# Performance work log

Measured on AMD Instinct MI355X. Metric: run time of the kernel, lower is better.

Reference implementation:

```python
import jax, jax.numpy as jnp
import numpy as np

HIDDEN = 2048
N_HEADS = 16
HEAD_DIM = HIDDEN // N_HEADS  # 128
BATCH = 2
SEQ = 2048


def setup_inputs() -> dict:
    key = jax.random.key(0)
    ks = jax.random.split(key, 9)
    std = HIDDEN ** -0.5
    inp = {
        "hidden_states": jax.random.normal(ks[0], (BATCH, SEQ, HIDDEN), dtype=jnp.float32),
        "q_w": jax.random.normal(ks[1], (HIDDEN, HIDDEN), dtype=jnp.float32) * std,
        "k_w": jax.random.normal(ks[2], (HIDDEN, HIDDEN), dtype=jnp.float32) * std,
        "v_w": jax.random.normal(ks[3], (HIDDEN, HIDDEN), dtype=jnp.float32) * std,
        "o_w": jax.random.normal(ks[4], (HIDDEN, HIDDEN), dtype=jnp.float32) * std,
        "q_b": jnp.zeros((HIDDEN,), dtype=jnp.float32),
        "k_b": jnp.zeros((HIDDEN,), dtype=jnp.float32),
        "v_b": jnp.zeros((HIDDEN,), dtype=jnp.float32),
        "o_b": jnp.zeros((HIDDEN,), dtype=jnp.float32),
    }
    return inp


def reference(hidden_states, q_w, k_w, v_w, o_w, q_b, k_b, v_b, o_b):
    b, s, _ = hidden_states.shape
    # Projections (nn.Linear applies x @ W^T + b); split heads -> [b, h, s, d]
    def proj(w, bias):
        y = hidden_states @ w.T + bias
        return y.reshape(b, s, N_HEADS, HEAD_DIM).transpose(0, 2, 1, 3)

    q = proj(q_w, q_b)
    k = proj(k_w, k_b)
    v = proj(v_w, v_b)

    scale = 1.0 / jnp.sqrt(jnp.float32(HEAD_DIM))
    scores = jnp.einsum("bhqd,bhkd->bhqk", q, k) * scale  # [b, h, s, s]

    # causal mask: mask positions where k > q (triu, diagonal=1)
    qi = jnp.arange(s)[:, None]
    ki = jnp.arange(s)[None, :]
    scores = jnp.where(ki > qi, -jnp.inf, scores)

    attn = jax.nn.softmax(scores.astype(jnp.float32), axis=-1).astype(q.dtype)
    out = jnp.einsum("bhqk,bhkd->bhqd", attn, v)
    out = out.transpose(0, 2, 1, 3).reshape(b, s, HIDDEN)
    return out @ o_w.T + o_b
```

## Files before the change

### kernel.cpp

```cpp
#include <hip/hip_runtime.h>

#define S_HID 2048
#define S_SEQ 2048
#define S_B   2
#define S_NH  16
#define S_HD  128
#define S_M   (S_B * S_SEQ)
#define S_BH  (S_B * S_NH)

typedef __bf16 bf16_t;
typedef __bf16 bf16x8 __attribute__((ext_vector_type(8)));
typedef __bf16 bf16x4 __attribute__((ext_vector_type(4)));
typedef float  floatx4 __attribute__((ext_vector_type(4)));
typedef float  floatx16 __attribute__((ext_vector_type(16)));

typedef __attribute__((address_space(1))) unsigned int as1_uint;
typedef __attribute__((address_space(3))) unsigned int as3_uint;

__device__ __forceinline__ void gload_lds16(const void* g, void* l) {
    __builtin_amdgcn_global_load_lds((as1_uint*)g, (as3_uint*)l, 16, 0, 0);
}

__global__ void cvt_all(const float* __restrict__ x,
                        const float* __restrict__ qw, const float* __restrict__ kw,
                        const float* __restrict__ vw, const float* __restrict__ ow,
                        bf16_t* __restrict__ Xb, bf16_t* __restrict__ Wqkv) {
    const int XV = (S_M * S_HID) >> 2;
    const int WV = (S_HID * S_HID) >> 2;
    const int total = XV + 4 * WV;
    int stride = gridDim.x * blockDim.x;
    for (int i = blockIdx.x * blockDim.x + threadIdx.x; i < total; i += stride) {
        const float* src;
        bf16x4* dst;
        int local;
        if (i < XV) {
            src = x; local = i; dst = (bf16x4*)Xb;
        } else {
            int j = i - XV;
            int r = j >> 20;
            local = j & (WV - 1);
            src = r == 0 ? qw : r == 1 ? kw : r == 2 ? vw : ow;
            dst = (bf16x4*)Wqkv + (size_t)r * WV;
        }
        float4 v = ((const float4*)src)[local];
        bf16x4 o;
        o.x = (bf16_t)v.x; o.y = (bf16_t)v.y; o.z = (bf16_t)v.z; o.w = (bf16_t)v.w;
        dst[local] = o;
    }
}

__global__ __launch_bounds__(256, 4)
void gemm_qkv(const bf16_t* __restrict__ A, const bf16_t* __restrict__ W,
              const float* __restrict__ qbias, const float* __restrict__ kbias,
              const float* __restrict__ vbias,
              bf16_t* __restrict__ Qo, bf16_t* __restrict__ Ko, bf16_t* __restrict__ Vto,
              float qscale) {
    __shared__ __align__(16) bf16_t ldsA[128 * 64];
    __shared__ __align__(16) bf16_t ldsB[128 * 64];
    const int tid = threadIdx.x;
    const int wid = tid >> 6, lane = tid & 63;
    const int m0 = blockIdx.y * 128, n0 = blockIdx.x * 128;
    const int wm = (wid & 1) * 64, wn = (wid >> 1) * 64;
    const int lm = lane & 15, quad = lane >> 4;
    const int srow = lane >> 3;
    const int scol = lane & 7;

    floatx4 acc[4][4];
    #pragma unroll
    for (int i = 0; i < 4; ++i)
        #pragma unroll
        for (int j = 0; j < 4; ++j)
            acc[i][j] = (floatx4){0.f, 0.f, 0.f, 0.f};

    for (int kt = 0; kt < S_HID; kt += 64) {
        #pragma unroll
        for (int i = 0; i < 4; ++i) {
            int slot = i * 4 + wid;
            int row = slot * 8 + srow;
            int cg = scol ^ (row & 7);
            gload_lds16(A + (size_t)(m0 + row) * S_HID + kt + cg * 8, &ldsA[slot * 512]);
            gload_lds16(W + (size_t)(n0 + row) * S_HID + kt + cg * 8, &ldsB[slot * 512]);
        }
        __syncthreads();
        #pragma unroll
        for (int k2 = 0; k2 < 2; ++k2) {
            bf16x8 af[4], bfr[4];
            #pragma unroll
            for (int i = 0; i < 4; ++i) {
                int row = wm + i * 16 + lm;
                int cc = (k2 * 4 + quad) ^ (row & 7);
                af[i] = *(const bf16x8*)&ldsA[row * 64 + cc * 8];
            }
            #pragma unroll
            for (int j = 0; j < 4; ++j) {
                int row = wn + j * 16 + lm;
                int cc = (k2 * 4 + quad) ^ (row & 7);
                bfr[j] = *(const bf16x8*)&ldsB[row * 64 + cc * 8];
            }
            #pragma unroll
            for (int i = 0; i < 4; ++i)
                #pragma unroll
                for (int j = 0; j < 4; ++j)
                    acc[i][j] = __builtin_amdgcn_mfma_f32_16x16x32_bf16(af[i], bfr[j], acc[i][j], 0, 0, 0);
        }
        __syncthreads();
    }

    const int region = n0 >> 11;
    if (region < 2) {
        bf16_t* Ob = region ? Ko : Qo;
        const float* bias = region ? kbias : qbias;
        float scale = region ? 1.0f : qscale;
        #pragma unroll
        for (int i = 0; i < 4; ++i) {
            #pragma unroll
            for (int j = 0; j < 4; ++j) {
                int n = n0 + wn + j * 16 + lm;
                float bv = bias[n & 2047];
                int nl = n & 2047;
                int h = nl >> 7, d = nl & 127;
                #pragma unroll
                for (int r = 0; r < 4; ++r) {
                    int m = m0 + wm + i * 16 + quad * 4 + r;
                    int b = m >> 11, s = m & 2047;
                    Ob[(((size_t)(b * S_NH + h)) * S_SEQ + s) * S_HD + d] =
                        (bf16_t)((acc[i][j][r] + bv) * scale);
                }
            }
        }
    } else {
        #pragma unroll
        for (int i = 0; i < 4; ++i) {
            #pragma unroll
            for (int j = 0; j < 4; ++j) {
                int n = n0 + wn + j * 16 + lm;
                int nl = n & 2047;
                float bv = vbias[nl];
                int h = nl >> 7, d = nl & 127;
                int m = m0 + wm + i * 16 + quad * 4;
                int b = m >> 11, s = m & 2047;
                bf16x4 ov;
                #pragma unroll
                for (int r = 0; r < 4; ++r) ov[r] = (bf16_t)(acc[i][j][r] + bv);
                *(bf16x4*)&Vto[(((size_t)(b * S_NH + h)) * S_HD + d) * S_SEQ + s] = ov;
            }
        }
    }
}

__global__ __launch_bounds__(256, 3)
void gemm_out(const bf16_t* __restrict__ A, const bf16_t* __restrict__ W,
              const float* __restrict__ bias, float* __restrict__ out) {
    __shared__ __align__(16) bf16_t ldsA[128 * 64];
    __shared__ __align__(16) bf16_t ldsB[128 * 64];
    const int tid = threadIdx.x;
    const int wid = tid >> 6, lane = tid & 63;
    const int m0 = blockIdx.y * 128, n0 = blockIdx.x * 128;
    const int wm = (wid & 1) * 64, wn = (wid >> 1) * 64;
    const int lm = lane & 15, quad = lane >> 4;
    const int srow = lane >> 3;
    const int scol = lane & 7;

    floatx4 acc[4][4];
    #pragma unroll
    for (int i = 0; i < 4; ++i)
        #pragma unroll
        for (int j = 0; j < 4; ++j)
            acc[i][j] = (floatx4){0.f, 0.f, 0.f, 0.f};

    for (int kt = 0; kt < S_HID; kt += 64) {
        #pragma unroll
        for (int i = 0; i < 4; ++i) {
            int slot = i * 4 + wid;
            int row = slot * 8 + srow;
            int cg = scol ^ (row & 7);
            gload_lds16(A + (size_t)(m0 + row) * S_HID + kt + cg * 8, &ldsA[slot * 512]);
            gload_lds16(W + (size_t)(n0 + row) * S_HID + kt + cg * 8, &ldsB[slot * 512]);
        }
        __syncthreads();
        #pragma unroll
        for (int k2 = 0; k2 < 2; ++k2) {
            bf16x8 af[4], bfr[4];
            #pragma unroll
            for (int i = 0; i < 4; ++i) {
                int row = wm + i * 16 + lm;
                int cc = (k2 * 4 + quad) ^ (row & 7);
                af[i] = *(const bf16x8*)&ldsA[row * 64 + cc * 8];
            }
            #pragma unroll
            for (int j = 0; j < 4; ++j) {
                int row = wn + j * 16 + lm;
                int cc = (k2 * 4 + quad) ^ (row & 7);
                bfr[j] = *(const bf16x8*)&ldsB[row * 64 + cc * 8];
            }
            #pragma unroll
            for (int i = 0; i < 4; ++i)
                #pragma unroll
                for (int j = 0; j < 4; ++j)
                    acc[i][j] = __builtin_amdgcn_mfma_f32_16x16x32_bf16(af[i], bfr[j], acc[i][j], 0, 0, 0);
        }
        __syncthreads();
    }

    #pragma unroll
    for (int i = 0; i < 4; ++i) {
        #pragma unroll
        for (int j = 0; j < 4; ++j) {
            int n = n0 + wn + j * 16 + lm;
            float bv = bias[n];
            #pragma unroll
            for (int r = 0; r < 4; ++r) {
                int m = m0 + wm + i * 16 + quad * 4 + r;
                out[(size_t)m * S_HID + n] = acc[i][j][r] + bv;
            }
        }
    }
}

__device__ __forceinline__ bf16x8 make_pfrag(bf16x4 lo, bf16x4 hi, int h) {
    int2 li = __builtin_bit_cast(int2, lo);
    int2 hh = __builtin_bit_cast(int2, hi);
    int2 xl, xh;
    xl.x = __shfl_xor(li.x, 32); xl.y = __shfl_xor(li.y, 32);
    xh.x = __shfl_xor(hh.x, 32); xh.y = __shfl_xor(hh.y, 32);
    int2 flo, fhi;
    flo.x = h ? xh.x : li.x;  flo.y = h ? xh.y : li.y;
    fhi.x = h ? hh.x : xl.x;  fhi.y = h ? hh.y : xl.y;
    bf16x4 a = __builtin_bit_cast(bf16x4, flo);
    bf16x4 b = __builtin_bit_cast(bf16x4, fhi);
    return __builtin_shufflevector(a, b, 0, 1, 2, 3, 4, 5, 6, 7);
}

__global__ __launch_bounds__(256, 2)
void attn(const bf16_t* __restrict__ Q, const bf16_t* __restrict__ K,
          const bf16_t* __restrict__ Vt, bf16_t* __restrict__ O) {
    __shared__ __align__(16) bf16_t ldsK[2][64 * 128];
    __shared__ __align__(16) bf16_t ldsV[2][128 * 64];
    const int tid = threadIdx.x, wid = tid >> 6, lane = tid & 63;
    const int lm = lane & 15, quad = lane >> 4;
    const int srow = lane >> 3, scol = lane & 7;
    const int c31 = lane & 31, h = lane >> 5, r7 = lane & 7;
    const int bx = blockIdx.x;
    const int bh = bx & 31, idx = bx >> 5;
    const int qt = idx < 8 ? idx : 23 - idx;
    const int q0 = qt * 128;
    const int b = bh >> 4, hd = bh & 15;

    const bf16_t* Kbase = K + (size_t)bh * S_SEQ * S_HD;
    const bf16_t* Vbase = Vt + (size_t)bh * S_HD * S_SEQ;

    const int qcol = q0 + wid * 32 + c31;
    const int nkt = qt * 2 + 2;

    bf16x8 qf[8];
    {
        const bf16_t* qp = Q + ((size_t)bh * S_SEQ + qcol) * S_HD + h * 8;
        #pragma unroll
        for (int ks = 0; ks < 8; ++ks) qf[ks] = *(const bf16x8*)(qp + ks * 16);
    }

    floatx16 oa[4];
    #pragma unroll
    for (int jd = 0; jd < 4; ++jd)
        #pragma unroll
        for (int e = 0; e < 16; ++e) oa[jd][e] = 0.f;
    float m_st = -1e30f, l_st = 0.f;

    #pragma unroll
    for (int i = 0; i < 4; ++i) {
        int slot = i * 4 + wid;
        int krow = slot * 4 + quad;
        int kcg = lm ^ (krow & 7);
        gload_lds16(Kbase + (size_t)krow * S_HD + kcg * 8, &ldsK[0][slot * 512]);
        int vrow = slot * 8 + srow;
        int vcg = scol ^ (vrow & 7);
        gload_lds16(Vbase + (size_t)vrow * S_SEQ + vcg * 8, &ldsV[0][slot * 512]);
    }

    int pp = 0;
    for (int kti = 0; kti < nkt; ++kti) {
        const int kt = kti * 64;
        __syncthreads();

        if (kti + 1 < nkt) {
            const int ktn = kt + 64;
            #pragma unroll
            for (int i = 0; i < 4; ++i) {
                int slot = i * 4 + wid;
                int krow = slot * 4 + quad;
                int kcg = lm ^ (krow & 7);
                gload_lds16(Kbase + (size_t)(ktn + krow) * S_HD + kcg * 8, &ldsK[pp ^ 1][slot * 512]);
                int vrow = slot * 8 + srow;
                int vcg = scol ^ (vrow & 7);
                gload_lds16(Vbase + (size_t)vrow * S_SEQ + ktn + vcg * 8, &ldsV[pp ^ 1][slot * 512]);
            }
        }

        floatx16 sa[2];
        #pragma unroll
        for (int jr = 0; jr < 2; ++jr)
            #pragma unroll
            for (int e = 0; e < 16; ++e) sa[jr][e] = 0.f;
        __builtin_amdgcn_s_setprio(1);
        #pragma unroll
        for (int ks = 0; ks < 8; ++ks) {
            #pragma unroll
            for (int jr = 0; jr < 2; ++jr) {
                int row = jr * 32 + c31;
                bf16x8 kf = *(const bf16x8*)&ldsK[pp][row * 128 + (((ks * 2 + h) ^ r7)) * 8];
                sa[jr] = __builtin_amdgcn_mfma_f32_32x32x16_bf16(kf, qf[ks], sa[jr], 0, 0, 0);
            }
        }
        __builtin_amdgcn_s_setprio(0);

        if (kti >= nkt - 2) {
            #pragma unroll
            for (int jr = 0; jr < 2; ++jr)
                #pragma unroll
                for (int rr = 0; rr < 16; ++rr) {
                    int key = kt + jr * 32 + (rr & 3) + 8 * (rr >> 2) + 4 * h;
                    if (key > qcol) sa[jr][rr] = -1e30f;
                }
        }

        float mx = -1e30f;
        #pragma unroll
        for (int jr = 0; jr < 2; ++jr)
            #pragma unroll
            for (int rr = 0; rr < 16; ++rr) mx = fmaxf(mx, sa[jr][rr]);
        mx = fmaxf(mx, __shfl_xor(mx, 32));
        float mn = fmaxf(m_st, mx);
        float al = __builtin_amdgcn_exp2f(m_st - mn);
        m_st = mn;

        float rs = 0.f;
        bf16x8 pf[4];
        #pragma unroll
        for (int jr = 0; jr < 2; ++jr) {
            bf16x4 pk[4];
            #pragma unroll
            for (int g = 0; g < 4; ++g)
                #pragma unroll
                for (int e = 0; e < 4; ++e) {
                    float p = __builtin_amdgcn_exp2f(sa[jr][g * 4 + e] - mn);
                    rs += p;
                    pk[g][e] = (bf16_t)p;
                }
            pf[jr * 2]     = make_pfrag(pk[0], pk[1], h);
            pf[jr * 2 + 1] = make_pfrag(pk[2], pk[3], h);
        }
        rs += __shfl_xor(rs, 32);
        l_st = l_st * al + rs;
        #pragma unroll
        for (int jd = 0; jd < 4; ++jd)
            #pragma unroll
            for (int e = 0; e < 16; ++e) oa[jd][e] *= al;

        __builtin_amdgcn_s_setprio(1);
        #pragma unroll
        for (int kb = 0; kb < 4; ++kb) {
            #pragma unroll
            for (int jd = 0; jd < 4; ++jd) {
                int row = jd * 32 + c31;
                bf16x8 vf = *(const bf16x8*)&ldsV[pp][row * 64 + (((kb * 2 + h) ^ r7)) * 8];
                oa[jd] = __builtin_amdgcn_mfma_f32_32x32x16_bf16(vf, pf[kb], oa[jd], 0, 0, 0);
            }
        }
        __builtin_amdgcn_s_setprio(0);
        pp ^= 1;
    }

    float inv = 1.0f / l_st;
    bf16_t* op = O + ((size_t)b * S_SEQ + qcol) * S_HID + hd * S_HD;
    #pragma unroll
    for (int jd = 0; jd < 4; ++jd)
        #pragma unroll
        for (int g = 0; g < 4; ++g) {
            bf16x4 ov;
            #pragma unroll
            for (int e = 0; e < 4; ++e) ov[e] = (bf16_t)(oa[jd][g * 4 + e] * inv);
            *(bf16x4*)&op[jd * 32 + g * 8 + 4 * h] = ov;
        }
}

extern "C" void kernel_launch(void* const* d_in, const int* in_sizes, int n_in,
                              void* d_out, int out_size, void* d_ws, size_t ws_size,
                              hipStream_t stream) {
    const float* hs = (const float*)d_in[0];
    const float* qw = (const float*)d_in[1];
    const float* kw = (const float*)d_in[2];
    const float* vw = (const float*)d_in[3];
    const float* ow = (const float*)d_in[4];
    const float* qbias = (const float*)d_in[5];
    const float* kbias = (const float*)d_in[6];
    const float* vbias = (const float*)d_in[7];
    const float* obias = (const float*)d_in[8];

    char* ws = (char*)d_ws;
    bf16_t* Xb   = (bf16_t*)(ws + 0);
    bf16_t* Wqkv = (bf16_t*)(ws + 16777216);
    bf16_t* Wob  = (bf16_t*)(ws + 41943040);
    bf16_t* Qb   = (bf16_t*)(ws + 50331648);
    bf16_t* Kb   = (bf16_t*)(ws + 67108864);
    bf16_t* Vtb  = (bf16_t*)(ws + 83886080);
    bf16_t* Ob   = Xb;

    cvt_all<<<2048, 256, 0, stream>>>(hs, qw, kw, vw, ow, Xb, Wqkv);

    const float qscale = 0.08838834764831845f * 1.4426950408889634f;
    gemm_qkv<<<dim3(48, 32), 256, 0, stream>>>(Xb, Wqkv, qbias, kbias, vbias,
                                               Qb, Kb, Vtb, qscale);

    attn<<<512, 256, 0, stream>>>(Qb, Kb, Vtb, Ob);

    gemm_out<<<dim3(16, 32), 256, 0, stream>>>(Ob, Wob, obias, (float*)d_out);
}
```

Before: 360.7 us.

## Triple-buffer QKV GEMM with 128x256 tiles and lazy softmax rescale in attention

The QKV projection GEMM moves to 512-thread blocks computing 128x256 tiles. A three-stage LDS ring buffer prefetches two K-steps ahead, the loads are interleaved across half-steps, and MFMA bursts run at raised priority. This is meant to overlap global loads with matrix math and cut the per-K-step full-sync stalls. Separately, the attention softmax skips the running-max update and the output rescale unless some lane's max grows by more than 8 in log2 units. That saves the rescale multiplies at the cost of slightly larger intermediate exponent values.

```diff
diff --git a/kernel.cpp b/kernel.cpp
--- a/kernel.cpp
+++ b/kernel.cpp
@@ -49,21 +49,23 @@
     }
 }
 
-__global__ __launch_bounds__(256, 4)
+__global__ __launch_bounds__(512, 2)
 void gemm_qkv(const bf16_t* __restrict__ A, const bf16_t* __restrict__ W,
               const float* __restrict__ qbias, const float* __restrict__ kbias,
               const float* __restrict__ vbias,
               bf16_t* __restrict__ Qo, bf16_t* __restrict__ Ko, bf16_t* __restrict__ Vto,
               float qscale) {
-    __shared__ __align__(16) bf16_t ldsA[128 * 64];
-    __shared__ __align__(16) bf16_t ldsB[128 * 64];
+    __shared__ __align__(16) bf16_t ldsA[3][128 * 64];
+    __shared__ __align__(16) bf16_t ldsB[3][256 * 64];
     const int tid = threadIdx.x;
     const int wid = tid >> 6, lane = tid & 63;
-    const int m0 = blockIdx.y * 128, n0 = blockIdx.x * 128;
-    const int wm = (wid & 1) * 64, wn = (wid >> 1) * 64;
+    const int wr = wid >> 2, wc = wid & 3;
     const int lm = lane & 15, quad = lane >> 4;
-    const int srow = lane >> 3;
-    const int scol = lane & 7;
+    const int srow = lane >> 3, scol = lane & 7;
+    const int m0 = blockIdx.y * 128, n0 = blockIdx.x * 256;
+
+    const bf16_t* Ag = A + (size_t)m0 * S_HID;
+    const bf16_t* Wg = W + (size_t)n0 * S_HID;
 
     floatx4 acc[4][4];
     #pragma unroll
@@ -72,39 +74,76 @@
         for (int j = 0; j < 4; ++j)
             acc[i][j] = (floatx4){0.f, 0.f, 0.f, 0.f};
 
-    for (int kt = 0; kt < S_HID; kt += 64) {
-        #pragma unroll
-        for (int i = 0; i < 4; ++i) {
-            int slot = i * 4 + wid;
-            int row = slot * 8 + srow;
-            int cg = scol ^ (row & 7);
-            gload_lds16(A + (size_t)(m0 + row) * S_HID + kt + cg * 8, &ldsA[slot * 512]);
-            gload_lds16(W + (size_t)(n0 + row) * S_HID + kt + cg * 8, &ldsB[slot * 512]);
-        }
-        __syncthreads();
-        #pragma unroll
-        for (int k2 = 0; k2 < 2; ++k2) {
-            bf16x8 af[4], bfr[4];
-            #pragma unroll
-            for (int i = 0; i < 4; ++i) {
-                int row = wm + i * 16 + lm;
-                int cc = (k2 * 4 + quad) ^ (row & 7);
-                af[i] = *(const bf16x8*)&ldsA[row * 64 + cc * 8];
-            }
-            #pragma unroll
-            for (int j = 0; j < 4; ++j) {
-                int row = wn + j * 16 + lm;
-                int cc = (k2 * 4 + quad) ^ (row & 7);
-                bfr[j] = *(const bf16x8*)&ldsB[row * 64 + cc * 8];
-            }
-            #pragma unroll
-            for (int i = 0; i < 4; ++i)
-                #pragma unroll
-                for (int j = 0; j < 4; ++j)
-                    acc[i][j] = __builtin_amdgcn_mfma_f32_16x16x32_bf16(af[i], bfr[j], acc[i][j], 0, 0, 0);
-        }
-        __syncthreads();
-    }
+#define QKV_STAGE_A(BUF, KT) do {                                                     \
+        _Pragma("unroll")                                                             \
+        for (int r_ = 0; r_ < 2; ++r_) {                                              \
+            int row_ = (wid * 2 + r_) * 8 + srow;                                     \
+            int cg_ = scol ^ (row_ & 7);                                              \
+            gload_lds16(Ag + (size_t)row_ * S_HID + (KT) + cg_ * 8,                   \
+                        &ldsA[BUF][(wid * 2 + r_) * 512]);                            \
+        } } while (0)
+#define QKV_STAGE_B(BUF, KT, R0, R1) do {                                             \
+        _Pragma("unroll")                                                             \
+        for (int r_ = (R0); r_ < (R1); ++r_) {                                        \
+            int row_ = (wid * 4 + r_) * 8 + srow;                                     \
+            int cg_ = scol ^ (row_ & 7);                                              \
+            gload_lds16(Wg + (size_t)row_ * S_HID + (KT) + cg_ * 8,                   \
+                        &ldsB[BUF][(wid * 4 + r_) * 512]);                            \
+        } } while (0)
+#define QKV_MFMA16() do {                                                             \
+        __builtin_amdgcn_s_setprio(1);                                                \
+        _Pragma("unroll")                                                             \
+        for (int i_ = 0; i_ < 4; ++i_)                                                \
+            _Pragma("unroll")                                                         \
+            for (int j_ = 0; j_ < 4; ++j_)                                            \
+                acc[i_][j_] = __builtin_amdgcn_mfma_f32_16x16x32_bf16(                \
+                    af[i_], bfr[j_], acc[i_][j_], 0, 0, 0);                           \
+        __builtin_amdgcn_s_setprio(0);                                                \
+    } while (0)
+
+    const int x7 = lm & 7;
+    const int roA0 = (wr * 64 + lm) * 64;
+    const int roB0 = (wc * 64 + lm) * 64;
+    const int cc0 = (quad ^ x7) * 8;
+    const int cc1 = ((4 + quad) ^ x7) * 8;
+
+    QKV_STAGE_A(0, 0);  QKV_STAGE_B(0, 0, 0, 4);
+    QKV_STAGE_A(1, 64); QKV_STAGE_B(1, 64, 0, 4);
+    asm volatile("s_waitcnt vmcnt(6)" ::: "memory");
+    __builtin_amdgcn_s_barrier();
+
+    bf16x8 af[4], bfr[4];
+    int b0 = 0;
+    for (int t = 0; t < 32; ++t) {
+        int nb = b0 + 2; if (nb >= 3) nb -= 3;
+        const bool pf = (t + 2) < 32;
+        const int ktn = (t + 2) * 64;
+
+        #pragma unroll
+        for (int i = 0; i < 4; ++i) af[i] = *(const bf16x8*)&ldsA[b0][roA0 + i * 1024 + cc0];
+        #pragma unroll
+        for (int j = 0; j < 4; ++j) bfr[j] = *(const bf16x8*)&ldsB[b0][roB0 + j * 1024 + cc0];
+        if (pf) { QKV_STAGE_A(nb, ktn); QKV_STAGE_B(nb, ktn, 0, 1); }
+        __builtin_amdgcn_s_barrier();
+        QKV_MFMA16();
+        __builtin_amdgcn_s_barrier();
+
+        #pragma unroll
+        for (int i = 0; i < 4; ++i) af[i] = *(const bf16x8*)&ldsA[b0][roA0 + i * 1024 + cc1];
+        #pragma unroll
+        for (int j = 0; j < 4; ++j) bfr[j] = *(const bf16x8*)&ldsB[b0][roB0 + j * 1024 + cc1];
+        if (pf) { QKV_STAGE_B(nb, ktn, 1, 4); }
+        __builtin_amdgcn_s_barrier();
+        QKV_MFMA16();
+        if (t < 30)       asm volatile("s_waitcnt vmcnt(6)" ::: "memory");
+        else if (t == 30) asm volatile("s_waitcnt vmcnt(0)" ::: "memory");
+        __builtin_amdgcn_s_barrier();
+
+        b0 += 1; if (b0 == 3) b0 = 0;
+    }
+#undef QKV_STAGE_A
+#undef QKV_STAGE_B
+#undef QKV_MFMA16
 
     const int region = n0 >> 11;
     if (region < 2) {
@@ -115,15 +154,15 @@
         for (int i = 0; i < 4; ++i) {
             #pragma unroll
             for (int j = 0; j < 4; ++j) {
-                int n = n0 + wn + j * 16 + lm;
-                float bv = bias[n & 2047];
+                int n = n0 + wc * 64 + j * 16 + lm;
                 int nl = n & 2047;
+                float bv = bias[nl];
                 int h = nl >> 7, d = nl & 127;
                 #pragma unroll
                 for (int r = 0; r < 4; ++r) {
-                    int m = m0 + wm + i * 16 + quad * 4 + r;
-                    int b = m >> 11, s = m & 2047;
-                    Ob[(((size_t)(b * S_NH + h)) * S_SEQ + s) * S_HD + d] =
+                    int m = m0 + wr * 64 + i * 16 + quad * 4 + r;
+                    int bb = m >> 11, s = m & 2047;
+                    Ob[(((size_t)(bb * S_NH + h)) * S_SEQ + s) * S_HD + d] =
                         (bf16_t)((acc[i][j][r] + bv) * scale);
                 }
             }
@@ -133,16 +172,16 @@
         for (int i = 0; i < 4; ++i) {
             #pragma unroll
             for (int j = 0; j < 4; ++j) {
-                int n = n0 + wn + j * 16 + lm;
+                int n = n0 + wc * 64 + j * 16 + lm;
                 int nl = n & 2047;
                 float bv = vbias[nl];
                 int h = nl >> 7, d = nl & 127;
-                int m = m0 + wm + i * 16 + quad * 4;
-                int b = m >> 11, s = m & 2047;
+                int m = m0 + wr * 64 + i * 16 + quad * 4;
+                int bb = m >> 11, s = m & 2047;
                 bf16x4 ov;
                 #pragma unroll
                 for (int r = 0; r < 4; ++r) ov[r] = (bf16_t)(acc[i][j][r] + bv);
-                *(bf16x4*)&Vto[(((size_t)(b * S_NH + h)) * S_HD + d) * S_SEQ + s] = ov;
+                *(bf16x4*)&Vto[(((size_t)(bb * S_NH + h)) * S_HD + d) * S_SEQ + s] = ov;
             }
         }
     }
@@ -329,9 +368,17 @@
             #pragma unroll
             for (int rr = 0; rr < 16; ++rr) mx = fmaxf(mx, sa[jr][rr]);
         mx = fmaxf(mx, __shfl_xor(mx, 32));
-        float mn = fmaxf(m_st, mx);
-        float al = __builtin_amdgcn_exp2f(m_st - mn);
-        m_st = mn;
+
+        if (!__all(mx - m_st <= 8.0f)) {
+            float mn = fmaxf(m_st, mx);
+            float al = __builtin_amdgcn_exp2f(m_st - mn);
+            m_st = mn;
+            l_st *= al;
+            #pragma unroll
+            for (int jd = 0; jd < 4; ++jd)
+                #pragma unroll
+                for (int e = 0; e < 16; ++e) oa[jd][e] *= al;
+        }
 
         float rs = 0.f;
         bf16x8 pf[4];
@@ -342,7 +389,7 @@
             for (int g = 0; g < 4; ++g)
                 #pragma unroll
                 for (int e = 0; e < 4; ++e) {
-                    float p = __builtin_amdgcn_exp2f(sa[jr][g * 4 + e] - mn);
+                    float p = __builtin_amdgcn_exp2f(sa[jr][g * 4 + e] - m_st);
                     rs += p;
                     pk[g][e] = (bf16_t)p;
                 }
@@ -350,11 +397,7 @@
             pf[jr * 2 + 1] = make_pfrag(pk[2], pk[3], h);
         }
         rs += __shfl_xor(rs, 32);
-        l_st = l_st * al + rs;
-        #pragma unroll
-        for (int jd = 0; jd < 4; ++jd)
-            #pragma unroll
-            for (int e = 0; e < 16; ++e) oa[jd][e] *= al;
+        l_st += rs;
 
         __builtin_amdgcn_s_setprio(1);
         #pragma unroll
@@ -408,7 +451,7 @@
     cvt_all<<<2048, 256, 0, stream>>>(hs, qw, kw, vw, ow, Xb, Wqkv);
 
     const float qscale = 0.08838834764831845f * 1.4426950408889634f;
-    gemm_qkv<<<dim3(48, 32), 256, 0, stream>>>(Xb, Wqkv, qbias, kbias, vbias,
+    gemm_qkv<<<dim3(24, 32), 512, 0, stream>>>(Xb, Wqkv, qbias, kbias, vbias,
                                                Qb, Kb, Vtb, qscale);
 
     attn<<<512, 256, 0, stream>>>(Qb, Kb, Vtb, Ob);
```

After: 370.3 us. 1.03x slower.
